# Kernel tuning notes

Measured on AMD Instinct MI355X. Metric: run time of the kernel, lower is better.

The kernel has to match this reference:

```python
import jax, jax.numpy as jnp
import numpy as np

N, K = 262144, 8
IN_F, H_F, OUT_F = 16, 128, 16
NEG_SLOPE = 0.01  # torch LeakyReLU default


def setup_inputs() -> dict:
    key = jax.random.key(0)
    ks = jax.random.split(key, 10)
    h = jax.random.normal(ks[0], (N, IN_F), dtype=jnp.float32)
    pos = jax.random.uniform(ks[1], (N, 3), dtype=jnp.float32)
    nbr_idx = jax.random.randint(ks[2], (N, K), 0, N)

    def xavier(k, shape):
        fan_in, fan_out = shape[0], shape[1]
        a = jnp.sqrt(6.0 / (fan_in + fan_out))
        return jax.random.uniform(k, shape, jnp.float32, -a, a)

    W0 = xavier(ks[3], (K * IN_F, H_F))
    b0 = xavier(ks[4], (1, H_F))
    W1 = xavier(ks[5], (K * H_F, H_F))
    b1 = xavier(ks[6], (1, H_F))
    W2 = xavier(ks[7], (K * H_F, OUT_F))
    b2 = xavier(ks[8], (1, OUT_F))
    return {"h": h, "pos": pos, "nbr_idx": nbr_idx,
            "W0": W0, "b0": b0, "W1": W1, "b1": b1, "W2": W2, "b2": b2}


def _layer(h, pos, nbr_idx, W, b, activation):
    # gather neighbor messages and positions: [N, K, F], [N, K, 3]
    msgs = h[nbr_idx]
    src_pos = pos[nbr_idx]
    diff = pos[:, None, :] - src_pos                       # [N, K, 3]
    dist = jnp.sqrt(jnp.sum(diff * diff, axis=2, keepdims=True))  # [N, K, 1]
    dist = jnp.where(dist == 0, jnp.float32(0.5), dist)
    wow = (msgs / dist).reshape(h.shape[0], -1)            # [N, K*F]
    out = wow @ W + b
    if activation:
        out = jnp.where(out >= 0, out, NEG_SLOPE * out)
    return out


def reference(h, pos, nbr_idx, W0, b0, W1, b1, W2, b2):
    h1 = _layer(h, pos, nbr_idx, W0, b0, False)   # input layer
    h2 = _layer(h1, pos, nbr_idx, W1, b1, True)   # hidden layer (LeakyReLU)
    h3 = _layer(h2, pos, nbr_idx, W2, b2, False)  # output layer
    return h3
```

## Files before the change

### kernel.cpp

```cpp
#include <hip/hip_runtime.h>
#include <hip/hip_fp16.h>


typedef _Float16 f16x8 __attribute__((ext_vector_type(8)));
typedef float f32x4 __attribute__((ext_vector_type(4)));

#define NNODES 262144

__global__ __launch_bounds__(256) void prep_all_kernel(
    const float* __restrict__ W0, __half* __restrict__ W0f,
    const float* __restrict__ W1, __half* __restrict__ W1f,
    const float* __restrict__ W2, __half* __restrict__ W2f) {
    const int b = blockIdx.x;
    const int t = threadIdx.x;
    if (b < 64) {
        int e = b * 256 + t;
        int j = e & 7;
        int lane = (e >> 3) & 63;
        int rest = e >> 9;
        int tt = rest % 8;
        int s = rest / 8;
        int k = s * 32 + (lane >> 4) * 8 + j;
        int n = tt * 16 + (lane & 15);
        W0f[e] = __float2half(W0[k * 128 + n]);
    } else if (b < 576) {
        int e = (b - 64) * 256 + t;
        int j = e & 7;
        int lane = (e >> 3) & 63;
        int rest = e >> 9;
        int tt = rest % 8;
        int s = rest / 8;
        int k = s * 32 + (lane >> 4) * 8 + j;
        int n = tt * 16 + (lane & 15);
        W1f[e] = __float2half(W1[k * 128 + n]);
    } else {
        int e = (b - 576) * 256 + t;
        int j = e & 7;
        int lane = (e >> 3) & 63;
        int rest = e >> 9;
        int tt = rest % 8;
        int s = rest / 8;
        int k = s * 32 + (lane >> 4) * 8 + j;
        W2f[e] = __float2half(W2[(size_t)(tt * 128 + k) * 16 + (lane & 15)]);
    }
}

__global__ __launch_bounds__(256) void layer0_kernel(
    const float* __restrict__ h, const float* __restrict__ pos,
    const int* __restrict__ nbr, const __half* __restrict__ Wf,
    const float* __restrict__ bias, __half* __restrict__ invd,
    __half* __restrict__ outp) {
    __shared__ __align__(16) __half Bs[16384];

    const int tid = threadIdx.x;
    const int wave = tid >> 6;
    const int lane = tid & 63;
    const int quad = lane >> 4;
    const int lmod = lane & 15;
    const int mbase = blockIdx.x * 128 + wave * 16 + lmod;

    {
        const uint4* src = (const uint4*)Wf;
        uint4* dst = (uint4*)Bs;
#pragma unroll
        for (int i = 0; i < 8; ++i) dst[i * 256 + tid] = src[i * 256 + tid];
    }

    int idx[2][8];
#pragma unroll
    for (int mt = 0; mt < 2; ++mt) {
        const int m = mbase + mt * 64;
        const int4* nrow = (const int4*)(nbr + (size_t)m * 8);
        const int4 iA = nrow[0];
        const int4 iB = nrow[1];
        idx[mt][0] = iA.x; idx[mt][1] = iA.y; idx[mt][2] = iA.z; idx[mt][3] = iA.w;
        idx[mt][4] = iB.x; idx[mt][5] = iB.y; idx[mt][6] = iB.z; idx[mt][7] = iB.w;
    }

    f16x8 invr[2];
#pragma unroll
    for (int mt = 0; mt < 2; ++mt) {
        const int m = mbase + mt * 64;
        const float px = pos[m * 3 + 0];
        const float py = pos[m * 3 + 1];
        const float pz = pos[m * 3 + 2];
#pragma unroll
        for (int k = 0; k < 8; ++k) {
            const int n = idx[mt][k];
            const float dx = px - pos[n * 3 + 0];
            const float dy = py - pos[n * 3 + 1];
            const float dz = pz - pos[n * 3 + 2];
            float d = sqrtf(dx * dx + dy * dy + dz * dz);
            if (d == 0.0f) d = 0.5f;
            invr[mt][k] = (_Float16)((1.0f / d) * 0.00390625f);
        }
        if (quad == 0) *(f16x8*)(invd + (size_t)m * 8) = invr[mt];
    }

    f32x4 acc[2][8];
#pragma unroll
    for (int mt = 0; mt < 2; ++mt)
#pragma unroll
        for (int t = 0; t < 8; ++t) acc[mt][t] = f32x4{0.f, 0.f, 0.f, 0.f};

    __syncthreads();

#pragma unroll
    for (int s = 0; s < 4; ++s) {
        const int nb = 2 * s + (quad >> 1);
        f16x8 as[2];
#pragma unroll
        for (int mt = 0; mt < 2; ++mt) {
            const float* hp = h + (size_t)idx[mt][nb] * 16 + (quad & 1) * 8;
            const float4 f0 = *(const float4*)(hp);
            const float4 f1 = *(const float4*)(hp + 4);
            f16x8 av;
            av[0] = (_Float16)f0.x; av[1] = (_Float16)f0.y;
            av[2] = (_Float16)f0.z; av[3] = (_Float16)f0.w;
            av[4] = (_Float16)f1.x; av[5] = (_Float16)f1.y;
            av[6] = (_Float16)f1.z; av[7] = (_Float16)f1.w;
            as[mt] = av * invr[mt][nb];
        }
#pragma unroll
        for (int t = 0; t < 8; ++t) {
            f16x8 b = *(const f16x8*)(Bs + ((size_t)(s * 8 + t) * 64 + lane) * 8);
#pragma unroll
            for (int mt = 0; mt < 2; ++mt)
                acc[mt][t] = __builtin_amdgcn_mfma_f32_16x16x32_f16(as[mt], b, acc[mt][t], 0, 0, 0);
        }
    }

    __syncthreads();
#pragma unroll
    for (int mt = 0; mt < 2; ++mt) {
#pragma unroll
        for (int t = 0; t < 8; ++t) {
            const int col = t * 16 + lmod;
            const float bv = bias[col];
#pragma unroll
            for (int rr = 0; rr < 4; ++rr) {
                const int lrow = mt * 64 + wave * 16 + quad * 4 + rr;
                float v = acc[mt][t][rr] * 256.0f + bv;
                Bs[lrow * 128 + col] = __float2half(v);
            }
        }
    }
    __syncthreads();
    {
        const int lrow = tid >> 1;
        const int cb = (tid & 1) * 64;
        __half* gdst = outp + (size_t)(blockIdx.x * 128 + lrow) * 128 + cb;
        const __half* lsrc = Bs + lrow * 128 + cb;
#pragma unroll
        for (int j = 0; j < 8; ++j)
            *(f16x8*)(gdst + j * 8) = *(const f16x8*)(lsrc + j * 8);
    }
}

__device__ __forceinline__ int off16(int seg, int row) {
    return seg * 64 + (row & ~15) + ((row ^ seg) & 15);
}

__global__ __launch_bounds__(512, 4) void layer1p_kernel(
    const __half* __restrict__ hprev, const __half* __restrict__ invd,
    const int* __restrict__ nbr, const __half* __restrict__ Wf,
    const __half* __restrict__ Wf2s, const float* __restrict__ bias,
    __half* __restrict__ Pout) {
    __shared__ __align__(16) __half As[2][8192];

    const int tid = threadIdx.x;
    const int wave = tid >> 6;
    const int lane = tid & 63;
    const int quad = lane >> 4;
    const int lmod = lane & 15;
    const int rowblk = blockIdx.x * 64;
    const int seg = lmod;

    const int r0 = wave * 4 + quad;
    const int* nbp = nbr + (size_t)(rowblk + r0) * 8;
    const __half* ivp = invd + (size_t)(rowblk + r0) * 8;

    const int soff0 = off16(seg, r0) * 8;
    const int soff1 = off16(seg, r0 + 32) * 8;

    int roff4[4];
#pragma unroll
    for (int ks = 0; ks < 4; ++ks) {
        const int sg = ks * 4 + quad;
        roff4[ks] = (sg * 64 + ((lmod ^ sg) & 15)) * 8;
    }

    const __half* WfB = Wf + ((size_t)wave * 64 + lane) * 8;

    f16x8 Bc[2], Bn[2];
#pragma unroll
    for (int ks2 = 0; ks2 < 2; ++ks2)
        Bc[ks2] = *(const f16x8*)(WfB + (size_t)ks2 * 4096);

    f16x8 ga[2][2];
    {
        int id0[2], id1[2];
        id0[0] = nbp[0];   id0[1] = nbp[256];
        ga[0][0] = *(const f16x8*)(hprev + (size_t)id0[0] * 128 + seg * 8);
        ga[0][1] = *(const f16x8*)(hprev + (size_t)id0[1] * 128 + seg * 8);
        id1[0] = nbp[1];   id1[1] = nbp[257];
        ga[1][0] = *(const f16x8*)(hprev + (size_t)id1[0] * 128 + seg * 8);
        ga[1][1] = *(const f16x8*)(hprev + (size_t)id1[1] * 128 + seg * 8);
    }

    {
        const _Float16 s0 = *(const _Float16*)(ivp + 0);
        const _Float16 s1 = *(const _Float16*)(ivp + 256);
        *(f16x8*)(&As[0][soff0]) = ga[0][0] * s0;
        *(f16x8*)(&As[0][soff1]) = ga[0][1] * s1;
    }
    __syncthreads();

    f32x4 acc[4];
#pragma unroll
    for (int m = 0; m < 4; ++m) acc[m] = f32x4{0.f, 0.f, 0.f, 0.f};

#pragma unroll
    for (int nb = 0; nb < 8; ++nb) {
        const int cur = nb & 1;
        if (nb < 6) {
            int idn[2];
            idn[0] = nbp[nb + 2];
            idn[1] = nbp[nb + 258];
            ga[cur][0] = *(const f16x8*)(hprev + (size_t)idn[0] * 128 + seg * 8);
            ga[cur][1] = *(const f16x8*)(hprev + (size_t)idn[1] * 128 + seg * 8);
        }
#pragma unroll
        for (int h = 0; h < 2; ++h) {
            const int p = nb * 2 + h;
            if (p < 15) {
#pragma unroll
                for (int ks2 = 0; ks2 < 2; ++ks2)
                    Bn[ks2] = *(const f16x8*)(WfB + (size_t)((p + 1) * 2 + ks2) * 4096);
            }
#pragma unroll
            for (int m = 0; m < 4; ++m) {
#pragma unroll
                for (int ks2 = 0; ks2 < 2; ++ks2) {
                    f16x8 a = *(const f16x8*)(&As[cur][roff4[h * 2 + ks2] + m * 128]);
                    acc[m] = __builtin_amdgcn_mfma_f32_16x16x32_f16(a, Bc[ks2], acc[m], 0, 0, 0);
                }
            }
            Bc[0] = Bn[0];
            Bc[1] = Bn[1];
        }
        if (nb < 7) {
            const _Float16 s0 = *(const _Float16*)(ivp + nb + 1);
            const _Float16 s1 = *(const _Float16*)(ivp + nb + 257);
            *(f16x8*)(&As[cur ^ 1][soff0]) = ga[(nb + 1) & 1][0] * s0;
            *(f16x8*)(&As[cur ^ 1][soff1]) = ga[(nb + 1) & 1][1] * s1;
            __syncthreads();
        }
    }

    __half* As0 = &As[0][0];
    {
        const int col = wave * 16 + lmod;
        const float bv = bias[col];
        const int sg = col >> 3;
        const int jj = col & 7;
#pragma unroll
        for (int m = 0; m < 4; ++m) {
#pragma unroll
            for (int rr = 0; rr < 4; ++rr) {
                const int row = m * 16 + quad * 4 + rr;
                float v = acc[m][rr] * 256.0f + bv;
                v = (v >= 0.f) ? v : 0.01f * v;
                As0[off16(sg, row) * 8 + jj] = __float2half(v);
            }
        }
    }
    __syncthreads();

    const __half* WfB2 = Wf2s + ((size_t)wave * 64 + lane) * 8;
    f16x8 B2[4];
#pragma unroll
    for (int ks = 0; ks < 4; ++ks)
        B2[ks] = *(const f16x8*)(WfB2 + (size_t)ks * 4096);

    f32x4 acc2[4];
#pragma unroll
    for (int m = 0; m < 4; ++m) acc2[m] = f32x4{0.f, 0.f, 0.f, 0.f};
#pragma unroll
    for (int m = 0; m < 4; ++m) {
#pragma unroll
        for (int ks = 0; ks < 4; ++ks) {
            f16x8 a2 = *(const f16x8*)(&As0[roff4[ks] + m * 128]);
            acc2[m] = __builtin_amdgcn_mfma_f32_16x16x32_f16(a2, B2[ks], acc2[m], 0, 0, 0);
        }
    }

    {
        const int col = wave * 16 + lmod;
#pragma unroll
        for (int m = 0; m < 4; ++m) {
#pragma unroll
            for (int rr = 0; rr < 4; ++rr) {
                const int grow = rowblk + m * 16 + quad * 4 + rr;
                Pout[(size_t)grow * 128 + col] = __float2half(acc2[m][rr]);
            }
        }
    }
}

__global__ __launch_bounds__(256) void reduce_kernel(
    const __half* __restrict__ P, const __half* __restrict__ invd,
    const int* __restrict__ nbr, const float* __restrict__ b2,
    float* __restrict__ outp) {
    const int t = blockIdx.x * 256 + threadIdx.x;
    const int d = t >> 1;
    const int half = t & 1;

    const int4* nrow = (const int4*)(nbr + (size_t)d * 8);
    const int4 iA = nrow[0];
    const int4 iB = nrow[1];
    const int idx[8] = {iA.x, iA.y, iA.z, iA.w, iB.x, iB.y, iB.z, iB.w};
    const f16x8 iv = *(const f16x8*)(invd + (size_t)d * 8);

    f16x8 v[8];
#pragma unroll
    for (int k = 0; k < 8; ++k)
        v[k] = *(const f16x8*)(P + (size_t)idx[k] * 128 + k * 16 + half * 8);

    float acc[8];
#pragma unroll
    for (int c = 0; c < 8; ++c) acc[c] = 0.f;
#pragma unroll
    for (int k = 0; k < 8; ++k) {
        const float w = (float)iv[k];
#pragma unroll
        for (int c = 0; c < 8; ++c) acc[c] += w * (float)v[k][c];
    }

    const float* bp = b2 + half * 8;
    float4 o[2];
#pragma unroll
    for (int q = 0; q < 2; ++q) {
        o[q].x = acc[q * 4 + 0] * 256.0f + bp[q * 4 + 0];
        o[q].y = acc[q * 4 + 1] * 256.0f + bp[q * 4 + 1];
        o[q].z = acc[q * 4 + 2] * 256.0f + bp[q * 4 + 2];
        o[q].w = acc[q * 4 + 3] * 256.0f + bp[q * 4 + 3];
    }
    float4* dst = (float4*)(outp + (size_t)d * 16 + half * 8);
    dst[0] = o[0];
    dst[1] = o[1];
}

extern "C" void kernel_launch(void* const* d_in, const int* in_sizes, int n_in,
                              void* d_out, int out_size, void* d_ws, size_t ws_size,
                              hipStream_t stream) {
    const float* h   = (const float*)d_in[0];
    const float* pos = (const float*)d_in[1];
    const int*   nbr = (const int*)d_in[2];
    const float* W0  = (const float*)d_in[3];
    const float* b0  = (const float*)d_in[4];
    const float* W1  = (const float*)d_in[5];
    const float* b1  = (const float*)d_in[6];
    const float* W2  = (const float*)d_in[7];
    const float* b2  = (const float*)d_in[8];

    const int N = NNODES;

    char* w = (char*)d_ws;
    __half* h1 = (__half*)w;
    __half* P  = (__half*)(w + (size_t)67108864);
    __half* invd2 = (__half*)w;

    char* ob = (char*)d_out;
    __half* invd = (__half*)(ob + 0);
    __half* W0f  = (__half*)(ob + 4194304);
    __half* W1f  = (__half*)(ob + 4227072);
    __half* Wf2s = (__half*)(ob + 4489216);

    prep_all_kernel<<<640, 256, 0, stream>>>(W0, W0f, W1, W1f, W2, Wf2s);

    layer0_kernel<<<N / 128, 256, 0, stream>>>(h, pos, nbr, W0f, b0, invd, h1);
    layer1p_kernel<<<N / 64, 512, 0, stream>>>(h1, invd, nbr, W1f, Wf2s, b1, P);

    (void)hipMemcpyAsync(invd2, invd, 4194304, hipMemcpyDeviceToDevice, stream);

    reduce_kernel<<<(N * 2) / 256, 256, 0, stream>>>(P, invd2, nbr, b2, (float*)d_out);
}
```

Before: 313.5 us.

## Fuse weight prep into layer0 and split distance computation across quads

```diff
diff --git a/kernel.cpp b/kernel.cpp
--- a/kernel.cpp
+++ b/kernel.cpp
@@ -7,63 +7,64 @@
 
 #define NNODES 262144
 
-__global__ __launch_bounds__(256) void prep_all_kernel(
-    const float* __restrict__ W0, __half* __restrict__ W0f,
-    const float* __restrict__ W1, __half* __restrict__ W1f,
-    const float* __restrict__ W2, __half* __restrict__ W2f) {
-    const int b = blockIdx.x;
-    const int t = threadIdx.x;
-    if (b < 64) {
-        int e = b * 256 + t;
-        int j = e & 7;
-        int lane = (e >> 3) & 63;
-        int rest = e >> 9;
-        int tt = rest % 8;
-        int s = rest / 8;
-        int k = s * 32 + (lane >> 4) * 8 + j;
-        int n = tt * 16 + (lane & 15);
-        W0f[e] = __float2half(W0[k * 128 + n]);
-    } else if (b < 576) {
-        int e = (b - 64) * 256 + t;
-        int j = e & 7;
-        int lane = (e >> 3) & 63;
-        int rest = e >> 9;
-        int tt = rest % 8;
-        int s = rest / 8;
-        int k = s * 32 + (lane >> 4) * 8 + j;
-        int n = tt * 16 + (lane & 15);
-        W1f[e] = __float2half(W1[k * 128 + n]);
-    } else {
-        int e = (b - 576) * 256 + t;
-        int j = e & 7;
-        int lane = (e >> 3) & 63;
-        int rest = e >> 9;
-        int tt = rest % 8;
-        int s = rest / 8;
-        int k = s * 32 + (lane >> 4) * 8 + j;
-        W2f[e] = __float2half(W2[(size_t)(tt * 128 + k) * 16 + (lane & 15)]);
-    }
-}
-
 __global__ __launch_bounds__(256) void layer0_kernel(
     const float* __restrict__ h, const float* __restrict__ pos,
-    const int* __restrict__ nbr, const __half* __restrict__ Wf,
-    const float* __restrict__ bias, __half* __restrict__ invd,
-    __half* __restrict__ outp) {
+    const int* __restrict__ nbr,
+    const float* __restrict__ W0, const float* __restrict__ W1,
+    const float* __restrict__ W2, const float* __restrict__ bias,
+    __half* __restrict__ invd, __half* __restrict__ W1f,
+    __half* __restrict__ W2f, __half* __restrict__ outp) {
     __shared__ __align__(16) __half Bs[16384];
-
+    __shared__ __align__(16) __half exch[2][64][8];
+
+    const int b = blockIdx.x;
     const int tid = threadIdx.x;
+
+    if (b >= 2048) {
+        const int bb = b - 2048;
+        if (bb < 512) {
+            int e = bb * 256 + tid;
+            int j = e & 7;
+            int lane = (e >> 3) & 63;
+            int rest = e >> 9;
+            int tt = rest % 8;
+            int s = rest / 8;
+            int k = s * 32 + (lane >> 4) * 8 + j;
+            int n = tt * 16 + (lane & 15);
+            W1f[e] = __float2half(W1[k * 128 + n]);
+        } else {
+            int e = (bb - 512) * 256 + tid;
+            int j = e & 7;
+            int lane = (e >> 3) & 63;
+            int rest = e >> 9;
+            int tt = rest % 8;
+            int s = rest / 8;
+            int k = s * 32 + (lane >> 4) * 8 + j;
+            W2f[e] = __float2half(W2[(size_t)(tt * 128 + k) * 16 + (lane & 15)]);
+        }
+        return;
+    }
+
     const int wave = tid >> 6;
     const int lane = tid & 63;
     const int quad = lane >> 4;
     const int lmod = lane & 15;
-    const int mbase = blockIdx.x * 128 + wave * 16 + lmod;
-
-    {
-        const uint4* src = (const uint4*)Wf;
-        uint4* dst = (uint4*)Bs;
-#pragma unroll
-        for (int i = 0; i < 8; ++i) dst[i * 256 + tid] = src[i * 256 + tid];
+    const int mbase = b * 128 + wave * 16 + lmod;
+    const int grp = wave * 16 + lmod;
+
+    {
+#pragma unroll
+        for (int i = 0; i < 8; ++i) {
+            const int G = i * 256 + tid;
+            const int s = G >> 9;
+            const int t = (G >> 6) & 7;
+            const int ln = G & 63;
+            const float* wp = W0 + (size_t)(s * 32 + (ln >> 4) * 8) * 128 + t * 16 + (ln & 15);
+            f16x8 v;
+#pragma unroll
+            for (int j = 0; j < 8; ++j) v[j] = (_Float16)wp[j * 128];
+            *(f16x8*)(Bs + (size_t)G * 8) = v;
+        }
     }
 
     int idx[2][8];
@@ -77,7 +78,6 @@
         idx[mt][4] = iB.x; idx[mt][5] = iB.y; idx[mt][6] = iB.z; idx[mt][7] = iB.w;
     }
 
-    f16x8 invr[2];
 #pragma unroll
     for (int mt = 0; mt < 2; ++mt) {
         const int m = mbase + mt * 64;
@@ -85,16 +85,16 @@
         const float py = pos[m * 3 + 1];
         const float pz = pos[m * 3 + 2];
 #pragma unroll
-        for (int k = 0; k < 8; ++k) {
+        for (int kk = 0; kk < 2; ++kk) {
+            const int k = quad * 2 + kk;
             const int n = idx[mt][k];
             const float dx = px - pos[n * 3 + 0];
             const float dy = py - pos[n * 3 + 1];
             const float dz = pz - pos[n * 3 + 2];
             float d = sqrtf(dx * dx + dy * dy + dz * dz);
             if (d == 0.0f) d = 0.5f;
-            invr[mt][k] = (_Float16)((1.0f / d) * 0.00390625f);
-        }
-        if (quad == 0) *(f16x8*)(invd + (size_t)m * 8) = invr[mt];
+            exch[mt][grp][k] = (_Float16)((1.0f / d) * 0.00390625f);
+        }
     }
 
     f32x4 acc[2][8];
@@ -104,6 +104,13 @@
         for (int t = 0; t < 8; ++t) acc[mt][t] = f32x4{0.f, 0.f, 0.f, 0.f};
 
     __syncthreads();
+
+    f16x8 invr[2];
+#pragma unroll
+    for (int mt = 0; mt < 2; ++mt) {
+        invr[mt] = *(const f16x8*)&exch[mt][grp][0];
+        if (quad == 0) *(f16x8*)(invd + (size_t)(mbase + mt * 64) * 8) = invr[mt];
+    }
 
 #pragma unroll
     for (int s = 0; s < 4; ++s) {
@@ -123,10 +130,10 @@
         }
 #pragma unroll
         for (int t = 0; t < 8; ++t) {
-            f16x8 b = *(const f16x8*)(Bs + ((size_t)(s * 8 + t) * 64 + lane) * 8);
+            f16x8 bb = *(const f16x8*)(Bs + ((size_t)(s * 8 + t) * 64 + lane) * 8);
 #pragma unroll
             for (int mt = 0; mt < 2; ++mt)
-                acc[mt][t] = __builtin_amdgcn_mfma_f32_16x16x32_f16(as[mt], b, acc[mt][t], 0, 0, 0);
+                acc[mt][t] = __builtin_amdgcn_mfma_f32_16x16x32_f16(as[mt], bb, acc[mt][t], 0, 0, 0);
         }
     }
 
@@ -149,7 +156,7 @@
     {
         const int lrow = tid >> 1;
         const int cb = (tid & 1) * 64;
-        __half* gdst = outp + (size_t)(blockIdx.x * 128 + lrow) * 128 + cb;
+        __half* gdst = outp + (size_t)(b * 128 + lrow) * 128 + cb;
         const __half* lsrc = Bs + lrow * 128 + cb;
 #pragma unroll
         for (int j = 0; j < 8; ++j)
@@ -373,13 +380,11 @@
 
     char* ob = (char*)d_out;
     __half* invd = (__half*)(ob + 0);
-    __half* W0f  = (__half*)(ob + 4194304);
-    __half* W1f  = (__half*)(ob + 4227072);
-    __half* Wf2s = (__half*)(ob + 4489216);
-
-    prep_all_kernel<<<640, 256, 0, stream>>>(W0, W0f, W1, W1f, W2, Wf2s);
-
-    layer0_kernel<<<N / 128, 256, 0, stream>>>(h, pos, nbr, W0f, b0, invd, h1);
+    __half* W1f  = (__half*)(ob + 4194304);
+    __half* Wf2s = (__half*)(ob + 4456448);
+
+    layer0_kernel<<<2624, 256, 0, stream>>>(h, pos, nbr, W0, W1, W2, b0,
+                                            invd, W1f, Wf2s, h1);
     layer1p_kernel<<<N / 64, 512, 0, stream>>>(h1, invd, nbr, W1f, Wf2s, b1, P);
 
     (void)hipMemcpyAsync(invd2, invd, 4194304, hipMemcpyDeviceToDevice, stream);
```

Result: no change. 319.7 us (+2.0%).
